# Performance work log

Hardware: AMD Instinct MI355X
Metric: run time of the kernel (lower is better)

The kernel has to match this reference:

```python
import jax, jax.numpy as jnp
import numpy as np

P, H, T, B = 16, 24, 168, 4096


def _lstm(x, W_ih, W_hh, b_ih, b_hh):
    # x: [B, T, F]; PyTorch gate order i, f, g, o; returns all hidden states [B, T, H]
    Bsz = x.shape[0]
    Hd = W_hh.shape[1]
    # batch the input GEMM over all timesteps
    xg = jnp.einsum('btf,gf->btg', x, W_ih) + b_ih + b_hh  # [B, T, 4H]

    def step(carry, xt):
        h, c = carry
        g = xt + h @ W_hh.T  # [B, 4H]
        i, f, gg, o = jnp.split(g, 4, axis=-1)
        c = jax.nn.sigmoid(f) * c + jax.nn.sigmoid(i) * jnp.tanh(gg)
        h = jax.nn.sigmoid(o) * jnp.tanh(c)
        return (h, c), h

    h0 = jnp.zeros((Bsz, Hd), x.dtype)
    _, hs = jax.lax.scan(step, (h0, h0), jnp.swapaxes(xg, 0, 1))
    return jnp.swapaxes(hs, 0, 1)  # [B, T, H]


def setup_inputs() -> dict:
    key = jax.random.key(0)
    ks = jax.random.split(key, 14)
    s1 = 1.0 / np.sqrt(H)
    u = lambda k, shape: jax.random.uniform(k, shape, jnp.float32, -s1, s1)
    return {
        'x': jax.random.normal(ks[0], (B, T, P), jnp.float32),
        'W_ih1': u(ks[1], (4 * H, P)), 'W_hh1': u(ks[2], (4 * H, H)),
        'b_ih1': u(ks[3], (4 * H,)), 'b_hh1': u(ks[4], (4 * H,)),
        'W_ih2': u(ks[5], (4 * H, H)), 'W_hh2': u(ks[6], (4 * H, H)),
        'b_ih2': u(ks[7], (4 * H,)), 'b_hh2': u(ks[8], (4 * H,)),
        'W1': u(ks[9], (16, H)), 'b1': u(ks[10], (16,)),
        'W2': u(ks[11], (H, 16)), 'b2': u(ks[12], (H,)),
    }


def reference(x, W_ih1, W_hh1, b_ih1, b_hh1, W_ih2, W_hh2, b_ih2, b_hh2, W1, b1, W2, b2):
    h = jnp.tanh(_lstm(x, W_ih1, W_hh1, b_ih1, b_hh1))       # [B, T, H]
    h = jnp.tanh(_lstm(h, W_ih2, W_hh2, b_ih2, b_hh2))       # [B, T, H]
    h = h[:, -1, :]                                           # [B, H]
    h = jax.nn.relu(h @ W1.T + b1)                            # [B, 16]; dropout = identity (eval mode)
    out = h @ W2.T + b2                                       # [B, 24]
    return out.reshape(out.shape[0], -1, 1)                   # [B, 24, 1]
```

## Files before the change

### kernel.cpp

```cpp
#include <hip/hip_runtime.h>

constexpr int T = 168;
constexpr int P = 16;
constexpr int H = 24;

__device__ __forceinline__ float rcp_f(float x) { return __builtin_amdgcn_rcpf(x); }
__device__ __forceinline__ float sigm_f(float x) { return rcp_f(1.f + __expf(-x)); }
__device__ __forceinline__ float tanh_fast(float x) {
    return fmaf(2.f, rcp_f(1.f + __expf(-2.f * x)), -1.f);
}

#define LDS_SYNC() asm volatile("s_waitcnt lgkmcnt(0)" ::: "memory")

__global__ __attribute__((amdgpu_flat_work_group_size(64, 64),
                          amdgpu_waves_per_eu(2, 2)))
void lstm2_wave(const float* __restrict__ x,
                const float* __restrict__ Wih1, const float* __restrict__ Whh1,
                const float* __restrict__ bih1, const float* __restrict__ bhh1,
                const float* __restrict__ Wih2, const float* __restrict__ Whh2,
                const float* __restrict__ bih2, const float* __restrict__ bhh2,
                const float* __restrict__ W1, const float* __restrict__ b1,
                const float* __restrict__ W2, const float* __restrict__ b2,
                float* __restrict__ out)
{
    const int lane = threadIdx.x;
    const int s    = (lane < 48) ? lane : 47;
    const int u    = s % H;
    const int half = s / H;
    const int q0   = half * H + u;
    const int q1   = (2 + half) * H + u;
    const int row  = blockIdx.x;

    float wx0[P], wx1[P];
    float wh0[H], wh1[H];
    float vx0[H], vx1[H];
    float vh0[H], vh1[H];
    #pragma unroll
    for (int k = 0; k < P / 4; ++k) {
        float4 a = ((const float4*)(Wih1 + q0 * P))[k];
        float4 b = ((const float4*)(Wih1 + q1 * P))[k];
        wx0[4*k] = a.x; wx0[4*k+1] = a.y; wx0[4*k+2] = a.z; wx0[4*k+3] = a.w;
        wx1[4*k] = b.x; wx1[4*k+1] = b.y; wx1[4*k+2] = b.z; wx1[4*k+3] = b.w;
    }
    #pragma unroll
    for (int k = 0; k < H / 4; ++k) {
        float4 a = ((const float4*)(Whh1 + q0 * H))[k];
        float4 b = ((const float4*)(Whh1 + q1 * H))[k];
        wh0[4*k] = a.x; wh0[4*k+1] = a.y; wh0[4*k+2] = a.z; wh0[4*k+3] = a.w;
        wh1[4*k] = b.x; wh1[4*k+1] = b.y; wh1[4*k+2] = b.z; wh1[4*k+3] = b.w;
    }
    #pragma unroll
    for (int k = 0; k < H / 4; ++k) {
        float4 a = ((const float4*)(Wih2 + q0 * H))[k];
        float4 b = ((const float4*)(Wih2 + q1 * H))[k];
        vx0[4*k] = a.x; vx0[4*k+1] = a.y; vx0[4*k+2] = a.z; vx0[4*k+3] = a.w;
        vx1[4*k] = b.x; vx1[4*k+1] = b.y; vx1[4*k+2] = b.z; vx1[4*k+3] = b.w;
    }
    #pragma unroll
    for (int k = 0; k < H / 4; ++k) {
        float4 a = ((const float4*)(Whh2 + q0 * H))[k];
        float4 b = ((const float4*)(Whh2 + q1 * H))[k];
        vh0[4*k] = a.x; vh0[4*k+1] = a.y; vh0[4*k+2] = a.z; vh0[4*k+3] = a.w;
        vh1[4*k] = b.x; vh1[4*k+1] = b.y; vh1[4*k+2] = b.z; vh1[4*k+3] = b.w;
    }
    const float b10 = bih1[q0] + bhh1[q0];
    const float b11 = bih1[q1] + bhh1[q1];
    const float b20 = bih2[q0] + bhh2[q0];
    const float b21 = bih2[q1] + bhh2[q1];

    __shared__ __align__(16) float h1s[32];
    __shared__ __align__(16) float t1s[32];
    __shared__ __align__(16) float h2s[32];

    if (lane < H) { h1s[lane] = 0.f; t1s[lane] = 0.f; h2s[lane] = 0.f; }
    LDS_SYNC();

    const float* __restrict__ xrow = x + (size_t)row * T * P;

    float c1 = 0.f, c2 = 0.f;

    for (int t = 0; t < T; ++t) {
        float g0 = b10, g1 = b11;
        #pragma unroll
        for (int k = 0; k < P; ++k) {
            float xv = xrow[t * P + k];
            g0 = fmaf(xv, wx0[k], g0);
            g1 = fmaf(xv, wx1[k], g1);
        }
        #pragma unroll
        for (int k = 0; k < H / 4; ++k) {
            float4 hv = ((const float4*)h1s)[k];
            g0 = fmaf(hv.x, wh0[4*k],   g0);  g1 = fmaf(hv.x, wh1[4*k],   g1);
            g0 = fmaf(hv.y, wh0[4*k+1], g0);  g1 = fmaf(hv.y, wh1[4*k+1], g1);
            g0 = fmaf(hv.z, wh0[4*k+2], g0);  g1 = fmaf(hv.z, wh1[4*k+2], g1);
            g0 = fmaf(hv.w, wh0[4*k+3], g0);  g1 = fmaf(hv.w, wh1[4*k+3], g1);
        }
        float a0 = sigm_f(g0);
        float px = (half == 0) ? g1 + g1 : g1;
        float sv = sigm_f(px);
        float a1 = (half == 0) ? sv + sv - 1.f : sv;
        float fa = __shfl(a0, lane + 24);
        float oa = __shfl(a1, lane + 24);
        c1 = fmaf(fa, c1, a0 * a1);
        float h1 = oa * tanh_fast(c1);
        float th1 = tanh_fast(h1);
        if (lane < H) { h1s[lane] = h1; t1s[lane] = th1; }
        LDS_SYNC();

        float g2 = b20, g3 = b21;
        #pragma unroll
        for (int k = 0; k < H / 4; ++k) {
            float4 tv = ((const float4*)t1s)[k];
            g2 = fmaf(tv.x, vx0[4*k],   g2);  g3 = fmaf(tv.x, vx1[4*k],   g3);
            g2 = fmaf(tv.y, vx0[4*k+1], g2);  g3 = fmaf(tv.y, vx1[4*k+1], g3);
            g2 = fmaf(tv.z, vx0[4*k+2], g2);  g3 = fmaf(tv.z, vx1[4*k+2], g3);
            g2 = fmaf(tv.w, vx0[4*k+3], g2);  g3 = fmaf(tv.w, vx1[4*k+3], g3);
        }
        #pragma unroll
        for (int k = 0; k < H / 4; ++k) {
            float4 hv = ((const float4*)h2s)[k];
            g2 = fmaf(hv.x, vh0[4*k],   g2);  g3 = fmaf(hv.x, vh1[4*k],   g3);
            g2 = fmaf(hv.y, vh0[4*k+1], g2);  g3 = fmaf(hv.y, vh1[4*k+1], g3);
            g2 = fmaf(hv.z, vh0[4*k+2], g2);  g3 = fmaf(hv.z, vh1[4*k+2], g3);
            g2 = fmaf(hv.w, vh0[4*k+3], g2);  g3 = fmaf(hv.w, vh1[4*k+3], g3);
        }
        float a2 = sigm_f(g2);
        float py = (half == 0) ? g3 + g3 : g3;
        float sw = sigm_f(py);
        float a3 = (half == 0) ? sw + sw - 1.f : sw;
        float fb = __shfl(a2, lane + 24);
        float ob = __shfl(a3, lane + 24);
        c2 = fmaf(fb, c2, a2 * a3);
        float h2 = ob * tanh_fast(c2);
        if (lane < H) h2s[lane] = h2;
        LDS_SYNC();
    }

    if (lane < H) t1s[lane] = tanh_fast(h2s[lane]);
    LDS_SYNC();
    if (lane < 16) {
        float acc = b1[lane];
        #pragma unroll
        for (int j = 0; j < H; ++j) acc = fmaf(t1s[j], W1[lane * H + j], acc);
        h1s[lane] = fmaxf(acc, 0.f);
    }
    LDS_SYNC();
    if (lane < H) {
        float acc = b2[lane];
        #pragma unroll
        for (int j = 0; j < 16; ++j) acc = fmaf(h1s[j], W2[lane * 16 + j], acc);
        out[(size_t)row * H + lane] = acc;
    }
}

extern "C" void kernel_launch(void* const* d_in, const int* in_sizes, int n_in,
                              void* d_out, int out_size, void* d_ws, size_t ws_size,
                              hipStream_t stream)
{
    const float* x    = (const float*)d_in[0];
    const float* Wih1 = (const float*)d_in[1];
    const float* Whh1 = (const float*)d_in[2];
    const float* bih1 = (const float*)d_in[3];
    const float* bhh1 = (const float*)d_in[4];
    const float* Wih2 = (const float*)d_in[5];
    const float* Whh2 = (const float*)d_in[6];
    const float* bih2 = (const float*)d_in[7];
    const float* bhh2 = (const float*)d_in[8];
    const float* W1   = (const float*)d_in[9];
    const float* b1   = (const float*)d_in[10];
    const float* W2   = (const float*)d_in[11];
    const float* b2   = (const float*)d_in[12];
    float* out = (float*)d_out;

    const int B = in_sizes[0] / (T * P);
    hipLaunchKernelGGL(lstm2_wave, dim3(B), dim3(64), 0, stream,
                       x, Wih1, Whh1, bih1, bhh1, Wih2, Whh2, bih2, bhh2,
                       W1, b1, W2, b2, out);
}
```

Before: 448.7 us.

## Pipeline LSTM layers across two waves, processing four rows per block

Splits the two LSTM layers across two wavefronts in a 128-thread block. Layer 2 runs one timestep behind layer 1, exchanging data through double-buffered shared memory with a block barrier each step. Each block now handles four batch rows, so the weights held in registers are reused across rows, and x is prefetched into LDS one step ahead. The cost is a __syncthreads per timestep, one extra pipeline step, and a quarter as many blocks, which may lower the occupancy available to hide latency.

New measurement: 438.6 us. -2.2%, faster.

```diff
diff --git a/kernel.cpp b/kernel.cpp
--- a/kernel.cpp
+++ b/kernel.cpp
@@ -1,20 +1,21 @@
 #include <hip/hip_runtime.h>
 
-constexpr int T = 168;
-constexpr int P = 16;
-constexpr int H = 24;
+constexpr int T  = 168;
+constexpr int P  = 16;
+constexpr int H  = 24;
+constexpr int R  = 4;
+constexpr int K2 = 24;
 
 __device__ __forceinline__ float rcp_f(float x) { return __builtin_amdgcn_rcpf(x); }
 __device__ __forceinline__ float sigm_f(float x) { return rcp_f(1.f + __expf(-x)); }
 __device__ __forceinline__ float tanh_fast(float x) {
     return fmaf(2.f, rcp_f(1.f + __expf(-2.f * x)), -1.f);
 }
-
 #define LDS_SYNC() asm volatile("s_waitcnt lgkmcnt(0)" ::: "memory")
 
-__global__ __attribute__((amdgpu_flat_work_group_size(64, 64),
+__global__ __attribute__((amdgpu_flat_work_group_size(128, 128),
                           amdgpu_waves_per_eu(2, 2)))
-void lstm2_wave(const float* __restrict__ x,
+void lstm2_pipe(const float* __restrict__ x,
                 const float* __restrict__ Wih1, const float* __restrict__ Whh1,
                 const float* __restrict__ bih1, const float* __restrict__ bhh1,
                 const float* __restrict__ Wih2, const float* __restrict__ Whh2,
@@ -23,133 +24,164 @@
                 const float* __restrict__ W2, const float* __restrict__ b2,
                 float* __restrict__ out)
 {
-    const int lane = threadIdx.x;
+    const int tid  = threadIdx.x;
+    const int ph   = tid >> 6;
+    const int lane = tid & 63;
     const int s    = (lane < 48) ? lane : 47;
     const int u    = s % H;
     const int half = s / H;
     const int q0   = half * H + u;
     const int q1   = (2 + half) * H + u;
-    const int row  = blockIdx.x;
-
-    float wx0[P], wx1[P];
-    float wh0[H], wh1[H];
-    float vx0[H], vx1[H];
-    float vh0[H], vh1[H];
+    const int row0 = blockIdx.x * R;
+
+    __shared__ __align__(16) float xbuf[2][R][32];
+    __shared__ __align__(16) float t1b [2][R][32];
+    __shared__ __align__(16) float t2b [2][R][32];
+    __shared__ __align__(16) float h1s [R][32];
+    __shared__ __align__(16) float h2s [R][32];
+    __shared__ __align__(16) float hd  [R][16];
+
+    float wa0[K2], wa1[K2];
+    float wb0[K2], wb1[K2];
+    float bi0, bi1;
+    if (ph == 0) {
+        #pragma unroll
+        for (int k = 0; k < P / 4; ++k) {
+            float4 a = ((const float4*)(Wih1 + q0 * P))[k];
+            float4 b = ((const float4*)(Wih1 + q1 * P))[k];
+            wa0[4*k] = a.x; wa0[4*k+1] = a.y; wa0[4*k+2] = a.z; wa0[4*k+3] = a.w;
+            wa1[4*k] = b.x; wa1[4*k+1] = b.y; wa1[4*k+2] = b.z; wa1[4*k+3] = b.w;
+        }
+        #pragma unroll
+        for (int k = P; k < K2; ++k) { wa0[k] = 0.f; wa1[k] = 0.f; }
+        #pragma unroll
+        for (int k = 0; k < H / 4; ++k) {
+            float4 a = ((const float4*)(Whh1 + q0 * H))[k];
+            float4 b = ((const float4*)(Whh1 + q1 * H))[k];
+            wb0[4*k] = a.x; wb0[4*k+1] = a.y; wb0[4*k+2] = a.z; wb0[4*k+3] = a.w;
+            wb1[4*k] = b.x; wb1[4*k+1] = b.y; wb1[4*k+2] = b.z; wb1[4*k+3] = b.w;
+        }
+        bi0 = bih1[q0] + bhh1[q0];
+        bi1 = bih1[q1] + bhh1[q1];
+    } else {
+        #pragma unroll
+        for (int k = 0; k < H / 4; ++k) {
+            float4 a = ((const float4*)(Wih2 + q0 * H))[k];
+            float4 b = ((const float4*)(Wih2 + q1 * H))[k];
+            wa0[4*k] = a.x; wa0[4*k+1] = a.y; wa0[4*k+2] = a.z; wa0[4*k+3] = a.w;
+            wa1[4*k] = b.x; wa1[4*k+1] = b.y; wa1[4*k+2] = b.z; wa1[4*k+3] = b.w;
+        }
+        #pragma unroll
+        for (int k = 0; k < H / 4; ++k) {
+            float4 a = ((const float4*)(Whh2 + q0 * H))[k];
+            float4 b = ((const float4*)(Whh2 + q1 * H))[k];
+            wb0[4*k] = a.x; wb0[4*k+1] = a.y; wb0[4*k+2] = a.z; wb0[4*k+3] = a.w;
+            wb1[4*k] = b.x; wb1[4*k+1] = b.y; wb1[4*k+2] = b.z; wb1[4*k+3] = b.w;
+        }
+        bi0 = bih2[q0] + bhh2[q0];
+        bi1 = bih2[q1] + bhh2[q1];
+    }
+
+    if (ph == 0) {
+        if (lane < H) {
+            #pragma unroll
+            for (int r = 0; r < R; ++r) h1s[r][lane] = 0.f;
+        }
+        for (int f = lane; f < 128; f += 64) {
+            int p = f >> 6, rem = f & 63, r = rem >> 4, k = rem & 15;
+            xbuf[p][r][16 + k] = 0.f;
+        }
+        {
+            int rr = lane >> 4, kk = lane & 15;
+            xbuf[0][rr][kk] = x[(size_t)(row0 + rr) * T * P + kk];
+        }
+    } else {
+        if (lane < H) {
+            #pragma unroll
+            for (int r = 0; r < R; ++r) h2s[r][lane] = 0.f;
+        }
+    }
+    __syncthreads();
+
+    const float* in1base = (ph == 0) ? &xbuf[0][0][0] : &t1b[0][0][0];
+    float*       in2base = (ph == 0) ? &h1s[0][0]     : &h2s[0][0];
+    float*       outbase = (ph == 0) ? &t1b[0][0][0]  : &t2b[0][0][0];
+
+    float c[R];
     #pragma unroll
-    for (int k = 0; k < P / 4; ++k) {
-        float4 a = ((const float4*)(Wih1 + q0 * P))[k];
-        float4 b = ((const float4*)(Wih1 + q1 * P))[k];
-        wx0[4*k] = a.x; wx0[4*k+1] = a.y; wx0[4*k+2] = a.z; wx0[4*k+3] = a.w;
-        wx1[4*k] = b.x; wx1[4*k+1] = b.y; wx1[4*k+2] = b.z; wx1[4*k+3] = b.w;
-    }
-    #pragma unroll
-    for (int k = 0; k < H / 4; ++k) {
-        float4 a = ((const float4*)(Whh1 + q0 * H))[k];
-        float4 b = ((const float4*)(Whh1 + q1 * H))[k];
-        wh0[4*k] = a.x; wh0[4*k+1] = a.y; wh0[4*k+2] = a.z; wh0[4*k+3] = a.w;
-        wh1[4*k] = b.x; wh1[4*k+1] = b.y; wh1[4*k+2] = b.z; wh1[4*k+3] = b.w;
-    }
-    #pragma unroll
-    for (int k = 0; k < H / 4; ++k) {
-        float4 a = ((const float4*)(Wih2 + q0 * H))[k];
-        float4 b = ((const float4*)(Wih2 + q1 * H))[k];
-        vx0[4*k] = a.x; vx0[4*k+1] = a.y; vx0[4*k+2] = a.z; vx0[4*k+3] = a.w;
-        vx1[4*k] = b.x; vx1[4*k+1] = b.y; vx1[4*k+2] = b.z; vx1[4*k+3] = b.w;
-    }
-    #pragma unroll
-    for (int k = 0; k < H / 4; ++k) {
-        float4 a = ((const float4*)(Whh2 + q0 * H))[k];
-        float4 b = ((const float4*)(Whh2 + q1 * H))[k];
-        vh0[4*k] = a.x; vh0[4*k+1] = a.y; vh0[4*k+2] = a.z; vh0[4*k+3] = a.w;
-        vh1[4*k] = b.x; vh1[4*k+1] = b.y; vh1[4*k+2] = b.z; vh1[4*k+3] = b.w;
-    }
-    const float b10 = bih1[q0] + bhh1[q0];
-    const float b11 = bih1[q1] + bhh1[q1];
-    const float b20 = bih2[q0] + bhh2[q0];
-    const float b21 = bih2[q1] + bhh2[q1];
-
-    __shared__ __align__(16) float h1s[32];
-    __shared__ __align__(16) float t1s[32];
-    __shared__ __align__(16) float h2s[32];
-
-    if (lane < H) { h1s[lane] = 0.f; t1s[lane] = 0.f; h2s[lane] = 0.f; }
-    LDS_SYNC();
-
-    const float* __restrict__ xrow = x + (size_t)row * T * P;
-
-    float c1 = 0.f, c2 = 0.f;
-
-    for (int t = 0; t < T; ++t) {
-        float g0 = b10, g1 = b11;
-        #pragma unroll
-        for (int k = 0; k < P; ++k) {
-            float xv = xrow[t * P + k];
-            g0 = fmaf(xv, wx0[k], g0);
-            g1 = fmaf(xv, wx1[k], g1);
-        }
-        #pragma unroll
-        for (int k = 0; k < H / 4; ++k) {
-            float4 hv = ((const float4*)h1s)[k];
-            g0 = fmaf(hv.x, wh0[4*k],   g0);  g1 = fmaf(hv.x, wh1[4*k],   g1);
-            g0 = fmaf(hv.y, wh0[4*k+1], g0);  g1 = fmaf(hv.y, wh1[4*k+1], g1);
-            g0 = fmaf(hv.z, wh0[4*k+2], g0);  g1 = fmaf(hv.z, wh1[4*k+2], g1);
-            g0 = fmaf(hv.w, wh0[4*k+3], g0);  g1 = fmaf(hv.w, wh1[4*k+3], g1);
-        }
-        float a0 = sigm_f(g0);
-        float px = (half == 0) ? g1 + g1 : g1;
-        float sv = sigm_f(px);
-        float a1 = (half == 0) ? sv + sv - 1.f : sv;
-        float fa = __shfl(a0, lane + 24);
-        float oa = __shfl(a1, lane + 24);
-        c1 = fmaf(fa, c1, a0 * a1);
-        float h1 = oa * tanh_fast(c1);
-        float th1 = tanh_fast(h1);
-        if (lane < H) { h1s[lane] = h1; t1s[lane] = th1; }
-        LDS_SYNC();
-
-        float g2 = b20, g3 = b21;
-        #pragma unroll
-        for (int k = 0; k < H / 4; ++k) {
-            float4 tv = ((const float4*)t1s)[k];
-            g2 = fmaf(tv.x, vx0[4*k],   g2);  g3 = fmaf(tv.x, vx1[4*k],   g3);
-            g2 = fmaf(tv.y, vx0[4*k+1], g2);  g3 = fmaf(tv.y, vx1[4*k+1], g3);
-            g2 = fmaf(tv.z, vx0[4*k+2], g2);  g3 = fmaf(tv.z, vx1[4*k+2], g3);
-            g2 = fmaf(tv.w, vx0[4*k+3], g2);  g3 = fmaf(tv.w, vx1[4*k+3], g3);
-        }
-        #pragma unroll
-        for (int k = 0; k < H / 4; ++k) {
-            float4 hv = ((const float4*)h2s)[k];
-            g2 = fmaf(hv.x, vh0[4*k],   g2);  g3 = fmaf(hv.x, vh1[4*k],   g3);
-            g2 = fmaf(hv.y, vh0[4*k+1], g2);  g3 = fmaf(hv.y, vh1[4*k+1], g3);
-            g2 = fmaf(hv.z, vh0[4*k+2], g2);  g3 = fmaf(hv.z, vh1[4*k+2], g3);
-            g2 = fmaf(hv.w, vh0[4*k+3], g2);  g3 = fmaf(hv.w, vh1[4*k+3], g3);
-        }
-        float a2 = sigm_f(g2);
-        float py = (half == 0) ? g3 + g3 : g3;
-        float sw = sigm_f(py);
-        float a3 = (half == 0) ? sw + sw - 1.f : sw;
-        float fb = __shfl(a2, lane + 24);
-        float ob = __shfl(a3, lane + 24);
-        c2 = fmaf(fb, c2, a2 * a3);
-        float h2 = ob * tanh_fast(c2);
-        if (lane < H) h2s[lane] = h2;
-        LDS_SYNC();
-    }
-
-    if (lane < H) t1s[lane] = tanh_fast(h2s[lane]);
-    LDS_SYNC();
-    if (lane < 16) {
-        float acc = b1[lane];
-        #pragma unroll
-        for (int j = 0; j < H; ++j) acc = fmaf(t1s[j], W1[lane * H + j], acc);
-        h1s[lane] = fmaxf(acc, 0.f);
-    }
-    LDS_SYNC();
-    if (lane < H) {
-        float acc = b2[lane];
-        #pragma unroll
-        for (int j = 0; j < 16; ++j) acc = fmaf(h1s[j], W2[lane * 16 + j], acc);
-        out[(size_t)row * H + lane] = acc;
+    for (int r = 0; r < R; ++r) c[r] = 0.f;
+
+    for (int i = 0; i <= T; ++i) {
+        if ((unsigned)(i - ph) < (unsigned)T) {
+            const float* in1 = in1base + (size_t)((i + ph) & 1) * (R * 32);
+            float*       tou = outbase + (size_t)(i & 1) * (R * 32);
+            #pragma unroll
+            for (int r = 0; r < R; ++r) {
+                float g0 = bi0, g1 = bi1;
+                #pragma unroll
+                for (int k = 0; k < K2 / 4; ++k) {
+                    float4 a = ((const float4*)(in1 + r * 32))[k];
+                    float4 b = ((const float4*)(in2base + r * 32))[k];
+                    g0 = fmaf(a.x, wa0[4*k],   g0);  g1 = fmaf(a.x, wa1[4*k],   g1);
+                    g0 = fmaf(a.y, wa0[4*k+1], g0);  g1 = fmaf(a.y, wa1[4*k+1], g1);
+                    g0 = fmaf(a.z, wa0[4*k+2], g0);  g1 = fmaf(a.z, wa1[4*k+2], g1);
+                    g0 = fmaf(a.w, wa0[4*k+3], g0);  g1 = fmaf(a.w, wa1[4*k+3], g1);
+                    g0 = fmaf(b.x, wb0[4*k],   g0);  g1 = fmaf(b.x, wb1[4*k],   g1);
+                    g0 = fmaf(b.y, wb0[4*k+1], g0);  g1 = fmaf(b.y, wb1[4*k+1], g1);
+                    g0 = fmaf(b.z, wb0[4*k+2], g0);  g1 = fmaf(b.z, wb1[4*k+2], g1);
+                    g0 = fmaf(b.w, wb0[4*k+3], g0);  g1 = fmaf(b.w, wb1[4*k+3], g1);
+                }
+                float a0 = sigm_f(g0);
+                float px = (half == 0) ? g1 + g1 : g1;
+                float sv = sigm_f(px);
+                float a1 = (half == 0) ? sv + sv - 1.f : sv;
+                float fa = __shfl(a0, lane + 24);
+                float oa = __shfl(a1, lane + 24);
+                c[r] = fmaf(fa, c[r], a0 * a1);
+                float hv = oa * tanh_fast(c[r]);
+                float th = tanh_fast(hv);
+                if (lane < H) {
+                    *(in2base + r * 32 + lane) = hv;
+                    *(tou     + r * 32 + lane) = th;
+                }
+            }
+        }
+        if (ph == 0 && i + 1 < T) {
+            int rr = lane >> 4, kk = lane & 15;
+            xbuf[(i + 1) & 1][rr][kk] =
+                x[(size_t)(row0 + rr) * T * P + (size_t)(i + 1) * P + kk];
+        }
+        __syncthreads();
+    }
+
+    if (ph == 1) {
+        float w1r[H];
+        float w2r[16];
+        if (lane < 16) {
+            #pragma unroll
+            for (int j = 0; j < H; ++j) w1r[j] = W1[lane * H + j];
+        }
+        if (lane < H) {
+            #pragma unroll
+            for (int j = 0; j < 16; ++j) w2r[j] = W2[lane * 16 + j];
+        }
+        #pragma unroll
+        for (int r = 0; r < R; ++r) {
+            if (lane < 16) {
+                float acc = b1[lane];
+                #pragma unroll
+                for (int j = 0; j < H; ++j) acc = fmaf(t2b[0][r][j], w1r[j], acc);
+                hd[r][lane] = fmaxf(acc, 0.f);
+            }
+            LDS_SYNC();
+            if (lane < H) {
+                float acc = b2[lane];
+                #pragma unroll
+                for (int j = 0; j < 16; ++j) acc = fmaf(hd[r][j], w2r[j], acc);
+                out[(size_t)(row0 + r) * H + lane] = acc;
+            }
+            LDS_SYNC();
+        }
     }
 }
 
@@ -173,7 +205,7 @@
     float* out = (float*)d_out;
 
     const int B = in_sizes[0] / (T * P);
-    hipLaunchKernelGGL(lstm2_wave, dim3(B), dim3(64), 0, stream,
+    hipLaunchKernelGGL(lstm2_pipe, dim3(B / R), dim3(128), 0, stream,
                        x, Wih1, Whh1, bih1, bhh1, Wih2, Whh2, bih2, bhh2,
                        W1, b1, W2, b2, out);
 }
```

## Process four batch rows per wavefront to interleave independent LSTM recurrences

Applied to the files above, without the earlier changes.

Each 64-lane block now handles four batch rows instead of one. Their two-layer LSTM recurrences are interleaved in registers and in per-row LDS buffers, so the independent dependency chains can hide FMA, transcendental and LDS latency. The grid shrinks to B/4 blocks and occupancy is set to one wave per EU, which gives more registers for the per-row state. The explicit lgkmcnt wait is replaced by a compiler wave barrier, relying on the in-order LDS access of a single wave. In exchange each wave does four times the work serially, and the global x loads are still issued each timestep without prefetch.

Result: slower. 704.0 us (+56.9%).

```diff
diff --git a/kernel.cpp b/kernel.cpp
--- a/kernel.cpp
+++ b/kernel.cpp
@@ -3,25 +3,25 @@
 constexpr int T = 168;
 constexpr int P = 16;
 constexpr int H = 24;
+constexpr int R = 4;
 
 __device__ __forceinline__ float rcp_f(float x) { return __builtin_amdgcn_rcpf(x); }
 __device__ __forceinline__ float sigm_f(float x) { return rcp_f(1.f + __expf(-x)); }
 __device__ __forceinline__ float tanh_fast(float x) {
     return fmaf(2.f, rcp_f(1.f + __expf(-2.f * x)), -1.f);
 }
-
-#define LDS_SYNC() asm volatile("s_waitcnt lgkmcnt(0)" ::: "memory")
+#define WAVE_FENCE() __builtin_amdgcn_wave_barrier()
 
 __global__ __attribute__((amdgpu_flat_work_group_size(64, 64),
-                          amdgpu_waves_per_eu(2, 2)))
-void lstm2_wave(const float* __restrict__ x,
-                const float* __restrict__ Wih1, const float* __restrict__ Whh1,
-                const float* __restrict__ bih1, const float* __restrict__ bhh1,
-                const float* __restrict__ Wih2, const float* __restrict__ Whh2,
-                const float* __restrict__ bih2, const float* __restrict__ bhh2,
-                const float* __restrict__ W1, const float* __restrict__ b1,
-                const float* __restrict__ W2, const float* __restrict__ b2,
-                float* __restrict__ out)
+                          amdgpu_waves_per_eu(1, 1)))
+void lstm2_w4(const float* __restrict__ x,
+              const float* __restrict__ Wih1, const float* __restrict__ Whh1,
+              const float* __restrict__ bih1, const float* __restrict__ bhh1,
+              const float* __restrict__ Wih2, const float* __restrict__ Whh2,
+              const float* __restrict__ bih2, const float* __restrict__ bhh2,
+              const float* __restrict__ W1, const float* __restrict__ b1,
+              const float* __restrict__ W2, const float* __restrict__ b2,
+              float* __restrict__ out)
 {
     const int lane = threadIdx.x;
     const int s    = (lane < 48) ? lane : 47;
@@ -29,7 +29,7 @@
     const int half = s / H;
     const int q0   = half * H + u;
     const int q1   = (2 + half) * H + u;
-    const int row  = blockIdx.x;
+    const int row0 = blockIdx.x * R;
 
     float wx0[P], wx1[P];
     float wh0[H], wh1[H];
@@ -68,88 +68,128 @@
     const float b20 = bih2[q0] + bhh2[q0];
     const float b21 = bih2[q1] + bhh2[q1];
 
-    __shared__ __align__(16) float h1s[32];
-    __shared__ __align__(16) float t1s[32];
-    __shared__ __align__(16) float h2s[32];
-
-    if (lane < H) { h1s[lane] = 0.f; t1s[lane] = 0.f; h2s[lane] = 0.f; }
-    LDS_SYNC();
-
-    const float* __restrict__ xrow = x + (size_t)row * T * P;
-
-    float c1 = 0.f, c2 = 0.f;
+    __shared__ __align__(16) float h1s[R][32];
+    __shared__ __align__(16) float t1s[R][32];
+    __shared__ __align__(16) float h2s[R][32];
+
+    if (lane < H) {
+        #pragma unroll
+        for (int r = 0; r < R; ++r) { h1s[r][lane] = 0.f; h2s[r][lane] = 0.f; }
+    }
+    WAVE_FENCE();
+
+    float c1[R], c2[R];
+    #pragma unroll
+    for (int r = 0; r < R; ++r) { c1[r] = 0.f; c2[r] = 0.f; }
 
     for (int t = 0; t < T; ++t) {
-        float g0 = b10, g1 = b11;
-        #pragma unroll
-        for (int k = 0; k < P; ++k) {
-            float xv = xrow[t * P + k];
-            g0 = fmaf(xv, wx0[k], g0);
-            g1 = fmaf(xv, wx1[k], g1);
+        float g0[R], g1[R];
+        #pragma unroll
+        for (int r = 0; r < R; ++r) { g0[r] = b10; g1[r] = b11; }
+        #pragma unroll
+        for (int r = 0; r < R; ++r) {
+            const float* xp = x + ((size_t)(row0 + r) * T + t) * P;
+            #pragma unroll
+            for (int k = 0; k < P; ++k) {
+                float xv = xp[k];
+                g0[r] = fmaf(xv, wx0[k], g0[r]);
+                g1[r] = fmaf(xv, wx1[k], g1[r]);
+            }
         }
         #pragma unroll
         for (int k = 0; k < H / 4; ++k) {
-            float4 hv = ((const float4*)h1s)[k];
-            g0 = fmaf(hv.x, wh0[4*k],   g0);  g1 = fmaf(hv.x, wh1[4*k],   g1);
-            g0 = fmaf(hv.y, wh0[4*k+1], g0);  g1 = fmaf(hv.y, wh1[4*k+1], g1);
-            g0 = fmaf(hv.z, wh0[4*k+2], g0);  g1 = fmaf(hv.z, wh1[4*k+2], g1);
-            g0 = fmaf(hv.w, wh0[4*k+3], g0);  g1 = fmaf(hv.w, wh1[4*k+3], g1);
-        }
-        float a0 = sigm_f(g0);
-        float px = (half == 0) ? g1 + g1 : g1;
-        float sv = sigm_f(px);
-        float a1 = (half == 0) ? sv + sv - 1.f : sv;
-        float fa = __shfl(a0, lane + 24);
-        float oa = __shfl(a1, lane + 24);
-        c1 = fmaf(fa, c1, a0 * a1);
-        float h1 = oa * tanh_fast(c1);
-        float th1 = tanh_fast(h1);
-        if (lane < H) { h1s[lane] = h1; t1s[lane] = th1; }
-        LDS_SYNC();
-
-        float g2 = b20, g3 = b21;
+            float4 hv[R];
+            #pragma unroll
+            for (int r = 0; r < R; ++r) hv[r] = ((const float4*)h1s[r])[k];
+            #pragma unroll
+            for (int r = 0; r < R; ++r) {
+                g0[r] = fmaf(hv[r].x, wh0[4*k],   g0[r]);  g1[r] = fmaf(hv[r].x, wh1[4*k],   g1[r]);
+                g0[r] = fmaf(hv[r].y, wh0[4*k+1], g0[r]);  g1[r] = fmaf(hv[r].y, wh1[4*k+1], g1[r]);
+                g0[r] = fmaf(hv[r].z, wh0[4*k+2], g0[r]);  g1[r] = fmaf(hv[r].z, wh1[4*k+2], g1[r]);
+                g0[r] = fmaf(hv[r].w, wh0[4*k+3], g0[r]);  g1[r] = fmaf(hv[r].w, wh1[4*k+3], g1[r]);
+            }
+        }
+        #pragma unroll
+        for (int r = 0; r < R; ++r) {
+            float a0 = sigm_f(g0[r]);
+            float px = (half == 0) ? g1[r] + g1[r] : g1[r];
+            float sv = sigm_f(px);
+            float a1 = (half == 0) ? sv + sv - 1.f : sv;
+            float fa = __shfl(a0, lane + 24);
+            float oa = __shfl(a1, lane + 24);
+            c1[r] = fmaf(fa, c1[r], a0 * a1);
+            float hv = oa * tanh_fast(c1[r]);
+            float th = tanh_fast(hv);
+            if (lane < H) { h1s[r][lane] = hv; t1s[r][lane] = th; }
+        }
+        WAVE_FENCE();
+
+        float g2[R], g3[R];
+        #pragma unroll
+        for (int r = 0; r < R; ++r) { g2[r] = b20; g3[r] = b21; }
         #pragma unroll
         for (int k = 0; k < H / 4; ++k) {
-            float4 tv = ((const float4*)t1s)[k];
-            g2 = fmaf(tv.x, vx0[4*k],   g2);  g3 = fmaf(tv.x, vx1[4*k],   g3);
-            g2 = fmaf(tv.y, vx0[4*k+1], g2);  g3 = fmaf(tv.y, vx1[4*k+1], g3);
-            g2 = fmaf(tv.z, vx0[4*k+2], g2);  g3 = fmaf(tv.z, vx1[4*k+2], g3);
-            g2 = fmaf(tv.w, vx0[4*k+3], g2);  g3 = fmaf(tv.w, vx1[4*k+3], g3);
+            float4 tv[R];
+            #pragma unroll
+            for (int r = 0; r < R; ++r) tv[r] = ((const float4*)t1s[r])[k];
+            #pragma unroll
+            for (int r = 0; r < R; ++r) {
+                g2[r] = fmaf(tv[r].x, vx0[4*k],   g2[r]);  g3[r] = fmaf(tv[r].x, vx1[4*k],   g3[r]);
+                g2[r] = fmaf(tv[r].y, vx0[4*k+1], g2[r]);  g3[r] = fmaf(tv[r].y, vx1[4*k+1], g3[r]);
+                g2[r] = fmaf(tv[r].z, vx0[4*k+2], g2[r]);  g3[r] = fmaf(tv[r].z, vx1[4*k+2], g3[r]);
+                g2[r] = fmaf(tv[r].w, vx0[4*k+3], g2[r]);  g3[r] = fmaf(tv[r].w, vx1[4*k+3], g3[r]);
+            }
         }
         #pragma unroll
         for (int k = 0; k < H / 4; ++k) {
-            float4 hv = ((const float4*)h2s)[k];
-            g2 = fmaf(hv.x, vh0[4*k],   g2);  g3 = fmaf(hv.x, vh1[4*k],   g3);
-            g2 = fmaf(hv.y, vh0[4*k+1], g2);  g3 = fmaf(hv.y, vh1[4*k+1], g3);
-            g2 = fmaf(hv.z, vh0[4*k+2], g2);  g3 = fmaf(hv.z, vh1[4*k+2], g3);
-            g2 = fmaf(hv.w, vh0[4*k+3], g2);  g3 = fmaf(hv.w, vh1[4*k+3], g3);
-        }
-        float a2 = sigm_f(g2);
-        float py = (half == 0) ? g3 + g3 : g3;
-        float sw = sigm_f(py);
-        float a3 = (half == 0) ? sw + sw - 1.f : sw;
-        float fb = __shfl(a2, lane + 24);
-        float ob = __shfl(a3, lane + 24);
-        c2 = fmaf(fb, c2, a2 * a3);
-        float h2 = ob * tanh_fast(c2);
-        if (lane < H) h2s[lane] = h2;
-        LDS_SYNC();
-    }
-
-    if (lane < H) t1s[lane] = tanh_fast(h2s[lane]);
-    LDS_SYNC();
+            float4 hv[R];
+            #pragma unroll
+            for (int r = 0; r < R; ++r) hv[r] = ((const float4*)h2s[r])[k];
+            #pragma unroll
+            for (int r = 0; r < R; ++r) {
+                g2[r] = fmaf(hv[r].x, vh0[4*k],   g2[r]);  g3[r] = fmaf(hv[r].x, vh1[4*k],   g3[r]);
+                g2[r] = fmaf(hv[r].y, vh0[4*k+1], g2[r]);  g3[r] = fmaf(hv[r].y, vh1[4*k+1], g3[r]);
+                g2[r] = fmaf(hv[r].z, vh0[4*k+2], g2[r]);  g3[r] = fmaf(hv[r].z, vh1[4*k+2], g3[r]);
+                g2[r] = fmaf(hv[r].w, vh0[4*k+3], g2[r]);  g3[r] = fmaf(hv[r].w, vh1[4*k+3], g3[r]);
+            }
+        }
+        #pragma unroll
+        for (int r = 0; r < R; ++r) {
+            float a2 = sigm_f(g2[r]);
+            float py = (half == 0) ? g3[r] + g3[r] : g3[r];
+            float sw = sigm_f(py);
+            float a3 = (half == 0) ? sw + sw - 1.f : sw;
+            float fb = __shfl(a2, lane + 24);
+            float ob = __shfl(a3, lane + 24);
+            c2[r] = fmaf(fb, c2[r], a2 * a3);
+            if (lane < H) h2s[r][lane] = ob * tanh_fast(c2[r]);
+        }
+        WAVE_FENCE();
+    }
+
+    if (lane < H) {
+        #pragma unroll
+        for (int r = 0; r < R; ++r) t1s[r][lane] = tanh_fast(h2s[r][lane]);
+    }
+    WAVE_FENCE();
     if (lane < 16) {
-        float acc = b1[lane];
-        #pragma unroll
-        for (int j = 0; j < H; ++j) acc = fmaf(t1s[j], W1[lane * H + j], acc);
-        h1s[lane] = fmaxf(acc, 0.f);
-    }
-    LDS_SYNC();
+        #pragma unroll
+        for (int r = 0; r < R; ++r) {
+            float acc = b1[lane];
+            #pragma unroll
+            for (int j = 0; j < H; ++j) acc = fmaf(t1s[r][j], W1[lane * H + j], acc);
+            h1s[r][lane] = fmaxf(acc, 0.f);
+        }
+    }
+    WAVE_FENCE();
     if (lane < H) {
-        float acc = b2[lane];
-        #pragma unroll
-        for (int j = 0; j < 16; ++j) acc = fmaf(h1s[j], W2[lane * 16 + j], acc);
-        out[(size_t)row * H + lane] = acc;
+        #pragma unroll
+        for (int r = 0; r < R; ++r) {
+            float acc = b2[lane];
+            #pragma unroll
+            for (int j = 0; j < 16; ++j) acc = fmaf(h1s[r][j], W2[lane * 16 + j], acc);
+            out[(size_t)(row0 + r) * H + lane] = acc;
+        }
     }
 }
 
@@ -173,7 +213,7 @@
     float* out = (float*)d_out;
 
     const int B = in_sizes[0] / (T * P);
-    hipLaunchKernelGGL(lstm2_wave, dim3(B), dim3(64), 0, stream,
+    hipLaunchKernelGGL(lstm2_w4, dim3(B / R), dim3(64), 0, stream,
                        x, Wih1, Whh1, bih1, bhh1, Wih2, Whh2, bih2, bhh2,
                        W1, b1, W2, b2, out);
 }
```
